# Performance work log

Measured on AMD Instinct MI355X. Metric: run time of the kernel, lower is better.

The kernel has to match this reference:

```python
import jax, jax.numpy as jnp
import numpy as np

B, L, H, E = 4, 2048, 8, 64
WINDOW = 8
DILATION = 1


def setup_inputs() -> dict:
    key = jax.random.key(0)
    kq, kk, kv, ka = jax.random.split(key, 4)
    queries = jax.random.normal(kq, (B, L, H, E), dtype=jnp.float32)
    keys = jax.random.normal(kk, (B, L, H, E), dtype=jnp.float32)
    values = jax.random.normal(kv, (B, L, H, E), dtype=jnp.float32)
    alpha = jax.random.uniform(ka, (1,), dtype=jnp.float32)
    return {"queries": queries, "keys": keys, "values": values, "alpha": alpha}


def _full_attention(q, k, v, scale):
    # q,k,v: [B, L, H, E]
    scores = jnp.einsum('blhe,bshe->bhls', q, k) * scale  # [B,H,L,L]
    A = jax.nn.softmax(scores, axis=-1)
    return jnp.einsum('bhls,bshd->blhd', A, v)


def _local_attention(q, k, v, scale):
    # efficient gather-based local window attention, non-causal
    Lk = k.shape[1]
    offsets = jnp.arange(-WINDOW, WINDOW + 1) * DILATION
    idx = jnp.clip(jnp.arange(Lk)[:, None] + offsets[None, :], 0, Lk - 1)
    K_win = k[:, idx]
    V_win = v[:, idx]
    scores = jnp.einsum('blhe,blwhe->blhw', q, K_win) * scale
    A = jax.nn.softmax(scores, axis=-1)
    return jnp.einsum('blhw,blwhe->blhe', A, V_win)


def reference(queries, keys, values, alpha):
    scale = 1.0 / np.sqrt(queries.shape[-1]).astype(np.float32)
    out_full = _full_attention(queries, keys, values, scale)
    out_local = _local_attention(queries, keys, values, scale)
    w = jax.nn.sigmoid(alpha[0])
    # only_target_first=True: positions 1..L-1 take out_full, position 0 is gated
    out = out_full.at[:, 0].set(w * out_full[:, 0] + (1.0 - w) * out_local[:, 0])
    return out
```

## Files before the change

### kernel.cpp

```cpp
#include <hip/hip_runtime.h>

typedef unsigned short u16;
typedef unsigned int   u32;
typedef __attribute__((ext_vector_type(8))) short short8;
typedef __attribute__((ext_vector_type(16))) float f32x16;

#define MFMA32(a, b, c) __builtin_amdgcn_mfma_f32_32x32x16_bf16(a, b, c, 0, 0, 0)

constexpr int Lv = 2048, Hv = 8, Ev = 64, HE = Hv * Ev;
constexpr float QSCALE = 0.18033688011112042f;
constexpr size_t WSV_OFF = 32u * 64u * 2048u;
#define WS_NEED ((size_t)16777216)

__device__ __forceinline__ float bf2f(u16 u) {
    u32 x = ((u32)u) << 16;
    return __builtin_bit_cast(float, x);
}
__device__ __forceinline__ u16 f2bf(float f) {
    u32 x = __builtin_bit_cast(u32, f);
    u32 r = ((x >> 16) & 1u) + 0x7fffu;
    return (u16)((x + r) >> 16);
}
__device__ __forceinline__ u32 pkbf(float a, float b) {
#if __has_builtin(__builtin_amdgcn_cvt_pk_bf16_f32)
    typedef __attribute__((ext_vector_type(2))) __bf16 bf16x2;
    bf16x2 v = __builtin_amdgcn_cvt_pk_bf16_f32(a, b);
    return __builtin_bit_cast(u32, v);
#else
    return (u32)f2bf(a) | ((u32)f2bf(b) << 16);
#endif
}
__device__ __forceinline__ float fexp2(float x) {
#if __has_builtin(__builtin_amdgcn_exp2f)
    return __builtin_amdgcn_exp2f(x);
#else
    return exp2f(x);
#endif
}

__device__ __forceinline__ int detect_isbf16(const u32* q32, int lane) {
    u32 w0 = q32[2 * lane];
    u32 w1 = q32[2 * lane + 1];
    u16 uu[4] = { (u16)(w0 & 0xffff), (u16)(w0 >> 16),
                  (u16)(w1 & 0xffff), (u16)(w1 >> 16) };
    int p = 0, z = 0;
#pragma unroll
    for (int j = 0; j < 4; ++j) {
        u16 mgn = (u16)(uu[j] & 0x7fff);
        int ex  = mgn >> 7;
        bool zero = (mgn == 0);
        bool pl   = zero || (ex >= 115 && ex <= 132);
        p += pl ? 1 : 0;
        if ((j & 1) == 0) z += zero ? 1 : 0;
    }
    int acc = p | (z << 16);
#pragma unroll
    for (int o = 1; o < 64; o <<= 1) acc += __shfl_xor(acc, o);
    int ps = acc & 0xffff, zs = acc >> 16;
    if (zs >= 100) return 0;
    return (ps >= 240) ? 1 : 0;
}

__device__ __forceinline__ short8 cvt8s(const float* p, float s) {
    float4 a = *(const float4*)p, b4 = *(const float4*)(p + 4);
    u32 r[4] = { pkbf(a.x * s, a.y * s), pkbf(a.z * s, a.w * s),
                 pkbf(b4.x * s, b4.y * s), pkbf(b4.z * s, b4.w * s) };
    return *(short8*)r;
}

__device__ __forceinline__ f32x16 zv16() {
    f32x16 z;
#pragma unroll
    for (int r = 0; r < 16; ++r) z[r] = 0.f;
    return z;
}

__device__ __forceinline__ void plswap(u32& a, u32& b) {
#if __has_builtin(__builtin_amdgcn_permlane32_swap)
    auto r = __builtin_amdgcn_permlane32_swap(a, b, false, false);
    a = r[0]; b = r[1];
#else
    int lane = (int)(threadIdx.x & 63);
    u32 ax = (u32)__shfl_xor((int)a, 32);
    u32 bx = (u32)__shfl_xor((int)b, 32);
    bool hi = lane >= 32;
    u32 na = hi ? bx : a;
    u32 nb = hi ? b  : ax;
    a = na; b = nb;
#endif
}

template <int ISBF>
__device__ __forceinline__ void convert_impl(const void* kin, const void* vin,
                                             u16* __restrict__ ws) {
    const int blk = blockIdx.x;
    const int bh  = blk >> 6, tg = blk & 63;
    const int b   = bh >> 3,  h  = bh & 7;
    const size_t inb = (size_t)b * Lv * HE + h * Ev;
    u16* kimg = ws + (size_t)blk * 2048;
    u16* vimg = ws + WSV_OFF + (size_t)blk * 2048;
    const int t = threadIdx.x;
#pragma unroll
    for (int r = 0; r < 4; ++r) {
        const int i = t + 256 * r;
        const int a = 2 * i;
        {
            int key = a >> 6;
            int slotf = (a & 63) >> 3, j0 = a & 7;
            int e0 = ((slotf ^ (key & 7)) << 3) + j0;
            size_t s = inb + (size_t)(tg * 32 + key) * HE + e0;
            u32 val;
            if (ISBF) { const u16* p = (const u16*)kin + s; val = (u32)p[0] | ((u32)p[1] << 16); }
            else      { const float* p = (const float*)kin + s; val = pkbf(p[0], p[1]); }
            *(u32*)&kimg[a] = val;
        }
        {
            int e = a >> 5;
            int slotf = (a & 31) >> 3, j0 = a & 7;
            int k0 = ((slotf ^ ((e + (e >> 3)) & 3)) << 3) + j0;
            size_t s0 = inb + (size_t)(tg * 32 + k0) * HE + e;
            u32 val;
            if (ISBF) { const u16* p = (const u16*)vin; val = (u32)p[s0] | ((u32)p[s0 + HE] << 16); }
            else      { const float* p = (const float*)vin; val = pkbf(p[s0], p[s0 + HE]); }
            *(u32*)&vimg[a] = val;
        }
    }
}

__global__ __launch_bounds__(256) void convert_kernel(
    const void* __restrict__ qv, const void* __restrict__ kv,
    const void* __restrict__ vv, u16* __restrict__ ws)
{
    const int isbf = detect_isbf16((const u32*)qv, threadIdx.x & 63);
    if (isbf) convert_impl<1>(kv, vv, ws);
    else      convert_impl<0>(kv, vv, ws);
}

template <int ISBF, int WS>
__device__ __forceinline__ void attn_impl(
    const void* __restrict__ qv, const void* __restrict__ kv,
    const void* __restrict__ vv, const void* __restrict__ alphav,
    void* __restrict__ outv, const u16* __restrict__ ws, u16* SMEM)
{
    const int tid  = threadIdx.x;
    const int w    = tid >> 6;
    const int lane = tid & 63;
    const int l31  = lane & 31;
    const int hi   = lane >> 5;
    const int qg   = w & 3;
    const int g    = w >> 2;

    const int fid = blockIdx.x;
    const int bh  = (fid & 7) * 4 + ((fid >> 3) & 3);
    const int rb  = fid >> 5;
    const int b   = bh >> 3, h = bh & 7;
    const int row0 = rb * 128;

    const size_t bhoff = (size_t)b * Lv * HE + h * Ev;
    const u16*   q16 = (const u16*)qv + bhoff;
    const u16*   k16 = (const u16*)kv + bhoff;
    const u16*   v16 = (const u16*)vv + bhoff;
    const float* q32 = (const float*)qv + bhoff;
    const float* k32 = (const float*)kv + bhoff;
    const float* v32 = (const float*)vv + bhoff;

    u16* ldsK = SMEM + w * 4096;
    u16* ldsV = ldsK + 2048;

    short8 qf[4];
    {
        size_t ro = (size_t)(row0 + qg * 32 + l31) * HE + hi * 8;
        if (ISBF) {
#pragma unroll
            for (int c = 0; c < 4; ++c) {
                short8 t = *(const short8*)(q16 + ro + 16 * c);
#pragma unroll
                for (int j = 0; j < 8; ++j)
                    qf[c][j] = (short)f2bf(bf2f((u16)t[j]) * QSCALE);
            }
        } else {
#pragma unroll
            for (int c = 0; c < 4; ++c) qf[c] = cvt8s(q32 + ro + 16 * c, QSCALE);
        }
    }

    f32x16 O[2];
    O[0] = zv16(); O[1] = zv16();
    float psum = 0.f;

    const u16* kimg0 = ws + ((size_t)bh * 64 + g * 32) * 2048;
    const u16* vimg0 = ws + WSV_OFF + ((size_t)bh * 64 + g * 32) * 2048;
    const size_t keybase = (size_t)g * 1024;

    const int k0l = lane >> 3;
    const int kj  = lane & 7;
    const int e0K = ((kj ^ k0l) << 3);
    const int eoV = kj * 8;

    uint4  kr0, kr1, kr2, kr3;
    float4 fpa, fpb, fpc, fpd;
    uint4  upa, upb;

#define LK1(KT) do { const u16* ib_ = kimg0 + (size_t)(KT) * 2048 + lane * 8;  \
        kr0 = *(const uint4*)ib_;        kr1 = *(const uint4*)(ib_ + 512);     \
        kr2 = *(const uint4*)(ib_ + 1024); kr3 = *(const uint4*)(ib_ + 1536); } while (0)
#define SK1() do { *(uint4*)&ldsK[lane * 8] = kr0;                             \
        *(uint4*)&ldsK[512 + lane * 8] = kr1;                                  \
        *(uint4*)&ldsK[1024 + lane * 8] = kr2;                                 \
        *(uint4*)&ldsK[1536 + lane * 8] = kr3; } while (0)
#define LV1(KT) do { const u16* ib_ = vimg0 + (size_t)(KT) * 2048 + lane * 8;  \
        kr0 = *(const uint4*)ib_;        kr1 = *(const uint4*)(ib_ + 512);     \
        kr2 = *(const uint4*)(ib_ + 1024); kr3 = *(const uint4*)(ib_ + 1536); } while (0)
#define SV1() do { *(uint4*)&ldsV[lane * 8] = kr0;                             \
        *(uint4*)&ldsV[512 + lane * 8] = kr1;                                  \
        *(uint4*)&ldsV[1024 + lane * 8] = kr2;                                 \
        *(uint4*)&ldsV[1536 + lane * 8] = kr3; } while (0)

#define LK0(KT, CH) do {                                                       \
        size_t tb_ = (keybase + (size_t)(KT) * 32) * HE;                       \
        int key_ = (CH) * 16 + k0l;                                            \
        if (ISBF) {                                                            \
            const u16* p_ = k16 + tb_ + (size_t)key_ * HE + e0K;               \
            upa = *(const uint4*)p_;                                           \
            upb = *(const uint4*)(p_ + 8 * HE);                                \
        } else {                                                               \
            const float* p_ = k32 + tb_ + (size_t)key_ * HE + e0K;             \
            fpa = *(const float4*)p_;            fpb = *(const float4*)(p_ + 4);\
            fpc = *(const float4*)(p_ + 8 * HE); fpd = *(const float4*)(p_ + 8 * HE + 4);\
        }                                                                      \
    } while (0)
#define SK0(CH) do {                                                           \
        if (ISBF) {                                                            \
            *(uint4*)&ldsK[((CH)*2    ) * 512 + lane * 8] = upa;               \
            *(uint4*)&ldsK[((CH)*2 + 1) * 512 + lane * 8] = upb;               \
        } else {                                                               \
            u32 t0_[4] = { pkbf(fpa.x, fpa.y), pkbf(fpa.z, fpa.w),             \
                           pkbf(fpb.x, fpb.y), pkbf(fpb.z, fpb.w) };           \
            u32 t1_[4] = { pkbf(fpc.x, fpc.y), pkbf(fpc.z, fpc.w),             \
                           pkbf(fpd.x, fpd.y), pkbf(fpd.z, fpd.w) };           \
            *(uint4*)&ldsK[((CH)*2    ) * 512 + lane * 8] = *(uint4*)t0_;      \
            *(uint4*)&ldsK[((CH)*2 + 1) * 512 + lane * 8] = *(uint4*)t1_;      \
        }                                                                      \
    } while (0)

#define LV0(KT, VH) do {                                                       \
        size_t tb_ = (keybase + (size_t)(KT) * 32 + (VH) * 16 + 2 * k0l) * HE; \
        if (ISBF) {                                                            \
            const u16* p_ = v16 + tb_ + eoV;                                   \
            upa = *(const uint4*)p_;                                           \
            upb = *(const uint4*)(p_ + HE);                                    \
        } else {                                                               \
            const float* p_ = v32 + tb_ + eoV;                                 \
            fpa = *(const float4*)p_;       fpb = *(const float4*)(p_ + 4);    \
            fpc = *(const float4*)(p_ + HE); fpd = *(const float4*)(p_ + HE + 4);\
        }                                                                      \
    } while (0)
#define SV0(VH) do {                                                           \
        int s_ = (k0l >> 2) + (VH) * 2;                                        \
        if (ISBF) {                                                            \
            const u16* a0_ = (const u16*)&upa;                                 \
            const u16* a1_ = (const u16*)&upb;                                 \
            _Pragma("unroll")                                                  \
            for (int j = 0; j < 8; ++j) {                                      \
                int e_ = eoV + j;                                              \
                int sl_ = s_ ^ ((e_ + (e_ >> 3)) & 3);                         \
                *(u32*)&ldsV[e_ * 32 + sl_ * 8 + ((2 * k0l) & 7)] =            \
                    (u32)a0_[j] | ((u32)a1_[j] << 16);                         \
            }                                                                  \
        } else {                                                               \
            float t0_[8] = {fpa.x, fpa.y, fpa.z, fpa.w, fpb.x, fpb.y, fpb.z, fpb.w};\
            float t1_[8] = {fpc.x, fpc.y, fpc.z, fpc.w, fpd.x, fpd.y, fpd.z, fpd.w};\
            _Pragma("unroll")                                                  \
            for (int j = 0; j < 8; ++j) {                                      \
                int e_ = eoV + j;                                              \
                int sl_ = s_ ^ ((e_ + (e_ >> 3)) & 3);                         \
                *(u32*)&ldsV[e_ * 32 + sl_ * 8 + ((2 * k0l) & 7)] =            \
                    pkbf(t0_[j], t1_[j]);                                      \
            }                                                                  \
        }                                                                      \
    } while (0)

    f32x16 St;
#define QK_() do {                                                             \
        St = zv16();                                                           \
        __builtin_amdgcn_s_setprio(1);                                         \
        _Pragma("unroll")                                                      \
        for (int c = 0; c < 4; ++c) {                                          \
            int sl = (2 * c + hi) ^ (l31 & 7);                                 \
            short8 kf = *(const short8*)&ldsK[l31 * 64 + sl * 8];              \
            St = MFMA32(kf, qf[c], St);                                        \
        }                                                                      \
        __builtin_amdgcn_s_setprio(0);                                         \
    } while (0)

    u32 c8[8];
#define SM_() do {                                                             \
        _Pragma("unroll")                                                      \
        for (int r = 0; r < 16; ++r) St[r] = fexp2(St[r]);                     \
        _Pragma("unroll")                                                      \
        for (int r = 0; r < 16; ++r) psum += St[r];                            \
        _Pragma("unroll")                                                      \
        for (int q = 0; q < 8; ++q) c8[q] = pkbf(St[2 * q], St[2 * q + 1]);    \
    } while (0)

#define PV_(T) do {                                                            \
        u32 a0 = c8[4 * (T) + 0], a1 = c8[4 * (T) + 1];                        \
        u32 a2 = c8[4 * (T) + 2], a3 = c8[4 * (T) + 3];                        \
        plswap(a0, a2);                                                        \
        plswap(a1, a3);                                                        \
        u32 pw_[4] = { a0, a1, a2, a3 };                                       \
        short8 pa = *(short8*)pw_;                                             \
        __builtin_amdgcn_s_setprio(1);                                         \
        _Pragma("unroll")                                                      \
        for (int et = 0; et < 2; ++et) {                                       \
            int e  = et * 32 + l31;                                            \
            int sl = (2 * (T) + hi) ^ ((e + (e >> 3)) & 3);                    \
            short8 vf = *(const short8*)&ldsV[e * 32 + sl * 8];                \
            O[et] = MFMA32(pa, vf, O[et]);                                     \
        }                                                                      \
        __builtin_amdgcn_s_setprio(0);                                         \
    } while (0)

    if (WS) {
        LK1(0); SK1(); LV1(0); SV1();
        for (int kt = 0; kt < 32; ++kt) {
            if (kt < 31) LK1(kt + 1);
            QK_();
            if (kt < 31) SK1();
            SM_();
            if (kt < 31) LV1(kt + 1);
            PV_(0);
            PV_(1);
            if (kt < 31) SV1();
        }
    } else {
        LK0(0, 0); SK0(0); LK0(0, 1); SK0(1);
        LV0(0, 0); SV0(0); LV0(0, 1); SV0(1);
        for (int kt = 0; kt < 32; ++kt) {
            if (kt < 31) LK0(kt + 1, 0);
            QK_();
            if (kt < 31) { SK0(0); LK0(kt + 1, 1); }
            SM_();
            if (kt < 31) { SK0(1); LV0(kt + 1, 0); }
            PV_(0);
            if (kt < 31) { SV0(0); LV0(kt + 1, 1); }
            PV_(1);
            if (kt < 31) SV0(1);
        }
    }
#undef LK1
#undef SK1
#undef LV1
#undef SV1
#undef LK0
#undef SK0
#undef LV0
#undef SV0
#undef QK_
#undef SM_
#undef PV_

    __syncthreads();
    float pst = psum + __shfl_xor(psum, 32);
    float* cb = (float*)SMEM;
    const int cbase = qg * 2368 + lane * 36;

    if (g == 1) {
        union { f32x16 v; float4 q4[4]; } u;
        u.v = O[0];
#pragma unroll
        for (int i = 0; i < 4; ++i) *(float4*)&cb[cbase + 4 * i] = u.q4[i];
        u.v = O[1];
#pragma unroll
        for (int i = 0; i < 4; ++i) *(float4*)&cb[cbase + 16 + 4 * i] = u.q4[i];
        cb[qg * 2368 + 2304 + lane] = pst;
    }

    float locv[2] = {0.f, 0.f};
    float wgt = 0.f;
    const bool w0blk = (rb == 0) && (w == 0);
    if (w0blk) {
        const int e = lane;
        const size_t base = bhoff + e;
#define LDIN(p, i) (ISBF ? bf2f(((const u16*)(p))[i]) : ((const float*)(p))[i])
        float qe = LDIN(qv, base);
        float s[9];
#pragma unroll
        for (int j = 0; j < 9; ++j) {
            float prod = qe * LDIN(kv, base + (size_t)j * HE);
#pragma unroll
            for (int o = 1; o < 64; o <<= 1) prod += __shfl_xor(prod, o);
            s[j] = prod * 0.125f;
        }
        float mx = s[0];
#pragma unroll
        for (int j = 1; j < 9; ++j) mx = fmaxf(mx, s[j]);
        float we[9];
#pragma unroll
        for (int j = 0; j < 9; ++j) we[j] = expf(s[j] - mx);
        float denom = 9.f * we[0];
        float acc   = 9.f * we[0] * LDIN(vv, base);
#pragma unroll
        for (int j = 1; j < 9; ++j) {
            denom += we[j];
            acc   += we[j] * LDIN(vv, base + (size_t)j * HE);
        }
        float loc = acc / denom;

        float a;
        if (ISBF) {
            a = bf2f(((const u16*)alphav)[0]);
            if (!(a >= 0.0f && a <= 1.0f)) {
                float af = ((const float*)alphav)[0];
                if (af >= 0.0f && af <= 1.0f) a = af;
            }
        } else {
            a = ((const float*)alphav)[0];
            if (!(a >= 0.0f && a <= 1.0f)) {
                float ab = bf2f(((const u16*)alphav)[0]);
                if (ab >= 0.0f && ab <= 1.0f) a = ab;
            }
        }
        wgt = 1.f / (1.f + expf(-a));
#pragma unroll
        for (int et = 0; et < 2; ++et) locv[et] = __shfl(loc, et * 32 + l31);
#undef LDIN
    }

    __syncthreads();
    if (g != 0) return;

    float pstp = cb[qg * 2368 + 2304 + lane];
#pragma unroll
    for (int r = 0; r < 16; ++r) {
        O[0][r] += cb[cbase + r];
        O[1][r] += cb[cbase + 16 + r];
    }
    float invv = 1.0f / (pst + pstp);

#pragma unroll
    for (int rg = 0; rg < 4; ++rg) {
#pragma unroll
        for (int rr = 0; rr < 4; ++rr) {
            const int reg = rg * 4 + rr;
            const int rl  = rr + 8 * rg + 4 * hi;
            float inv = __shfl(invv, rl);
            int row = row0 + qg * 32 + rl;
            size_t oo = (size_t)(b * Lv + row) * HE + h * Ev + l31;
            bool blend = w0blk && (rl == 0);
#pragma unroll
            for (int et = 0; et < 2; ++et) {
                float res = O[et][reg] * inv;
                if (blend) res = wgt * res + (1.f - wgt) * locv[et];
                if (ISBF) ((u16*)outv)[oo + et * 32] = f2bf(res);
                else      ((float*)outv)[oo + et * 32] = res;
            }
        }
    }
}

__global__ __launch_bounds__(512, 4) void attn_kernel_ws(
    const void* __restrict__ qv, const void* __restrict__ kv,
    const void* __restrict__ vv, const void* __restrict__ alphav,
    void* __restrict__ outv, const u16* __restrict__ ws)
{
    __shared__ u16 SMEM[32768];
    const int isbf = detect_isbf16((const u32*)qv, threadIdx.x & 63);
    if (isbf) attn_impl<1, 1>(qv, kv, vv, alphav, outv, ws, SMEM);
    else      attn_impl<0, 1>(qv, kv, vv, alphav, outv, ws, SMEM);
}

__global__ __launch_bounds__(512, 4) void attn_kernel_nws(
    const void* __restrict__ qv, const void* __restrict__ kv,
    const void* __restrict__ vv, const void* __restrict__ alphav,
    void* __restrict__ outv)
{
    __shared__ u16 SMEM[32768];
    const int isbf = detect_isbf16((const u32*)qv, threadIdx.x & 63);
    if (isbf) attn_impl<1, 0>(qv, kv, vv, alphav, outv, nullptr, SMEM);
    else      attn_impl<0, 0>(qv, kv, vv, alphav, outv, nullptr, SMEM);
}

extern "C" void kernel_launch(void* const* d_in, const int* in_sizes, int n_in,
                              void* d_out, int out_size, void* d_ws, size_t ws_size,
                              hipStream_t stream) {
    if (d_ws != nullptr && ws_size >= WS_NEED) {
        hipLaunchKernelGGL(convert_kernel, dim3(2048), dim3(256), 0, stream,
                           d_in[0], d_in[1], d_in[2], (u16*)d_ws);
        hipLaunchKernelGGL(attn_kernel_ws, dim3(512), dim3(512), 0, stream,
                           d_in[0], d_in[1], d_in[2], d_in[3], d_out,
                           (const u16*)d_ws);
    } else {
        hipLaunchKernelGGL(attn_kernel_nws, dim3(512), dim3(512), 0, stream,
                           d_in[0], d_in[1], d_in[2], d_in[3], d_out);
    }
}
```

Baseline: 155.4 us.

## Use direct global-to-LDS loads for K/V tiles and stage V transpose via LDS

The attention loop's K and V tile staging now uses global_load_lds, which writes straight into LDS instead of going through registers, with explicit vmcnt/lgkmcnt waits forming a pipeline. The last iteration is peeled out of the loop. The convert kernel now reads V with coalesced row loads into a padded LDS tile and transposes there, replacing strided scalar global reads. This is meant to cut register pressure and VGPR round trips in the main loop and to make the preprocessing reads coalesced. The hand-written waitcnt synchronisation is fragile: each wave fills only its own LDS buffers, so correctness depends on the wait placement.

```diff
diff --git a/kernel.cpp b/kernel.cpp
--- a/kernel.cpp
+++ b/kernel.cpp
@@ -36,6 +36,12 @@
 #else
     return exp2f(x);
 #endif
+}
+
+__device__ __forceinline__ void gll16(const void* g, void* l) {
+    __builtin_amdgcn_global_load_lds(
+        (const __attribute__((address_space(1))) void*)g,
+        (__attribute__((address_space(3))) void*)l, 16, 0, 0);
 }
 
 __device__ __forceinline__ int detect_isbf16(const u32* q32, int lane) {
@@ -92,7 +98,7 @@
 
 template <int ISBF>
 __device__ __forceinline__ void convert_impl(const void* kin, const void* vin,
-                                             u16* __restrict__ ws) {
+                                             u16* __restrict__ ws, u16* VT) {
     const int blk = blockIdx.x;
     const int bh  = blk >> 6, tg = blk & 63;
     const int b   = bh >> 3,  h  = bh & 7;
@@ -100,30 +106,44 @@
     u16* kimg = ws + (size_t)blk * 2048;
     u16* vimg = ws + WSV_OFF + (size_t)blk * 2048;
     const int t = threadIdx.x;
+
+#pragma unroll
+    for (int r = 0; r < 2; ++r) {
+        int f = t + 256 * r;
+        int key = f >> 4, part = f & 15;
+        size_t src = inb + (size_t)(tg * 32 + key) * HE + part * 4;
+        if (ISBF) {
+            uint2 vv_ = *(const uint2*)((const u16*)vin + src);
+            *(uint2*)&VT[key * 68 + part * 4] = vv_;
+        } else {
+            float4 v = *(const float4*)((const float*)vin + src);
+            *(u32*)&VT[key * 68 + part * 4]     = pkbf(v.x, v.y);
+            *(u32*)&VT[key * 68 + part * 4 + 2] = pkbf(v.z, v.w);
+        }
+    }
+
 #pragma unroll
     for (int r = 0; r < 4; ++r) {
-        const int i = t + 256 * r;
-        const int a = 2 * i;
-        {
-            int key = a >> 6;
-            int slotf = (a & 63) >> 3, j0 = a & 7;
-            int e0 = ((slotf ^ (key & 7)) << 3) + j0;
-            size_t s = inb + (size_t)(tg * 32 + key) * HE + e0;
-            u32 val;
-            if (ISBF) { const u16* p = (const u16*)kin + s; val = (u32)p[0] | ((u32)p[1] << 16); }
-            else      { const float* p = (const float*)kin + s; val = pkbf(p[0], p[1]); }
-            *(u32*)&kimg[a] = val;
-        }
-        {
-            int e = a >> 5;
-            int slotf = (a & 31) >> 3, j0 = a & 7;
-            int k0 = ((slotf ^ ((e + (e >> 3)) & 3)) << 3) + j0;
-            size_t s0 = inb + (size_t)(tg * 32 + k0) * HE + e;
-            u32 val;
-            if (ISBF) { const u16* p = (const u16*)vin; val = (u32)p[s0] | ((u32)p[s0 + HE] << 16); }
-            else      { const float* p = (const float*)vin; val = pkbf(p[s0], p[s0 + HE]); }
-            *(u32*)&vimg[a] = val;
-        }
+        int i = t + 256 * r, a = 2 * i;
+        int key = a >> 6, sf = (a & 63) >> 3, j0 = a & 7;
+        int e0 = ((sf ^ (key & 7)) << 3) + j0;
+        size_t s = inb + (size_t)(tg * 32 + key) * HE + e0;
+        u32 val;
+        if (ISBF) val = *(const u32*)((const u16*)kin + s);
+        else { float2 kvv = *(const float2*)((const float*)kin + s);
+               val = pkbf(kvv.x, kvv.y); }
+        *(u32*)&kimg[a] = val;
+    }
+
+    __syncthreads();
+
+#pragma unroll
+    for (int r = 0; r < 4; ++r) {
+        int i = t + 256 * r, a = 2 * i;
+        int e = a >> 5, sf = (a & 31) >> 3, j0 = a & 7;
+        int k0 = ((sf ^ ((e + (e >> 3)) & 3)) << 3) + j0;
+        u32 val = (u32)VT[k0 * 68 + e] | ((u32)VT[(k0 + 1) * 68 + e] << 16);
+        *(u32*)&vimg[a] = val;
     }
 }
 
@@ -131,9 +151,10 @@
     const void* __restrict__ qv, const void* __restrict__ kv,
     const void* __restrict__ vv, u16* __restrict__ ws)
 {
+    __shared__ u16 VT[32 * 68];
     const int isbf = detect_isbf16((const u32*)qv, threadIdx.x & 63);
-    if (isbf) convert_impl<1>(kv, vv, ws);
-    else      convert_impl<0>(kv, vv, ws);
+    if (isbf) convert_impl<1>(kv, vv, ws, VT);
+    else      convert_impl<0>(kv, vv, ws, VT);
 }
 
 template <int ISBF, int WS>
@@ -197,24 +218,27 @@
     const int e0K = ((kj ^ k0l) << 3);
     const int eoV = kj * 8;
 
-    uint4  kr0, kr1, kr2, kr3;
     float4 fpa, fpb, fpc, fpd;
     uint4  upa, upb;
 
-#define LK1(KT) do { const u16* ib_ = kimg0 + (size_t)(KT) * 2048 + lane * 8;  \
-        kr0 = *(const uint4*)ib_;        kr1 = *(const uint4*)(ib_ + 512);     \
-        kr2 = *(const uint4*)(ib_ + 1024); kr3 = *(const uint4*)(ib_ + 1536); } while (0)
-#define SK1() do { *(uint4*)&ldsK[lane * 8] = kr0;                             \
-        *(uint4*)&ldsK[512 + lane * 8] = kr1;                                  \
-        *(uint4*)&ldsK[1024 + lane * 8] = kr2;                                 \
-        *(uint4*)&ldsK[1536 + lane * 8] = kr3; } while (0)
-#define LV1(KT) do { const u16* ib_ = vimg0 + (size_t)(KT) * 2048 + lane * 8;  \
-        kr0 = *(const uint4*)ib_;        kr1 = *(const uint4*)(ib_ + 512);     \
-        kr2 = *(const uint4*)(ib_ + 1024); kr3 = *(const uint4*)(ib_ + 1536); } while (0)
-#define SV1() do { *(uint4*)&ldsV[lane * 8] = kr0;                             \
-        *(uint4*)&ldsV[512 + lane * 8] = kr1;                                  \
-        *(uint4*)&ldsV[1024 + lane * 8] = kr2;                                 \
-        *(uint4*)&ldsV[1536 + lane * 8] = kr3; } while (0)
+#define GLLK(KT) do {                                                          \
+        const u16* ib_ = kimg0 + (size_t)(KT) * 2048 + lane * 8;               \
+        _Pragma("unroll")                                                      \
+        for (int s_ = 0; s_ < 4; ++s_)                                         \
+            gll16(ib_ + s_ * 512, ldsK + s_ * 512);                            \
+    } while (0)
+#define GLLV(KT) do {                                                          \
+        const u16* ib_ = vimg0 + (size_t)(KT) * 2048 + lane * 8;               \
+        _Pragma("unroll")                                                      \
+        for (int s_ = 0; s_ < 4; ++s_)                                         \
+            gll16(ib_ + s_ * 512, ldsV + s_ * 512);                            \
+    } while (0)
+#define WAITV4() do { asm volatile("s_waitcnt vmcnt(4)" ::: "memory");         \
+        __builtin_amdgcn_sched_barrier(0); } while (0)
+#define WAITV0() do { asm volatile("s_waitcnt vmcnt(0)" ::: "memory");         \
+        __builtin_amdgcn_sched_barrier(0); } while (0)
+#define WAITL0() do { asm volatile("s_waitcnt lgkmcnt(0)" ::: "memory");       \
+        __builtin_amdgcn_sched_barrier(0); } while (0)
 
 #define LK0(KT, CH) do {                                                       \
         size_t tb_ = (keybase + (size_t)(KT) * 32) * HE;                       \
@@ -242,7 +266,6 @@
             *(uint4*)&ldsK[((CH)*2 + 1) * 512 + lane * 8] = *(uint4*)t1_;      \
         }                                                                      \
     } while (0)
-
 #define LV0(KT, VH) do {                                                       \
         size_t tb_ = (keybase + (size_t)(KT) * 32 + (VH) * 16 + 2 * k0l) * HE; \
         if (ISBF) {                                                            \
@@ -322,17 +345,24 @@
     } while (0)
 
     if (WS) {
-        LK1(0); SK1(); LV1(0); SV1();
-        for (int kt = 0; kt < 32; ++kt) {
-            if (kt < 31) LK1(kt + 1);
+        GLLK(0); GLLV(0);
+        for (int kt = 0; kt < 31; ++kt) {
+            WAITV4();
             QK_();
-            if (kt < 31) SK1();
+            WAITL0();
+            GLLK(kt + 1);
             SM_();
-            if (kt < 31) LV1(kt + 1);
+            WAITV4();
             PV_(0);
             PV_(1);
-            if (kt < 31) SV1();
-        }
+            WAITL0();
+            GLLV(kt + 1);
+        }
+        WAITV0();
+        QK_();
+        SM_();
+        PV_(0);
+        PV_(1);
     } else {
         LK0(0, 0); SK0(0); LK0(0, 1); SK0(1);
         LV0(0, 0); SV0(0); LV0(0, 1); SV0(1);
@@ -348,10 +378,11 @@
             if (kt < 31) SV0(1);
         }
     }
-#undef LK1
-#undef SK1
-#undef LV1
-#undef SV1
+#undef GLLK
+#undef GLLV
+#undef WAITV4
+#undef WAITV0
+#undef WAITL0
 #undef LK0
 #undef SK0
 #undef LV0
```

After: 150.0 us. 1.04x faster.
